# Kernel tuning notes

Hardware: AMD Instinct MI355X
Metric: run time of the kernel (lower is better)

## Reference

```python
import jax, jax.numpy as jnp
import numpy as np

HDIM = 4
P = 2 ** HDIM  # 16 hypercube nodes


def build_dense_weight(hweight, out_features, in_features):
    # hweight: [hdim+1, P, ob, ib]; assemble dense [out_features, in_features]
    ob = out_features // P
    ib = in_features // P
    i = jnp.arange(P)
    w = jnp.zeros((P, P, ob, ib), dtype=hweight.dtype)
    # diagonal blocks: w[i, i] = hweight[0, i]
    w = w.at[i, i].set(hweight[0])
    # hypercube neighbor blocks: w[i ^ (1<<d), i] = hweight[d+1, i]
    for d in range(HDIM):
        j = i ^ (1 << d)
        w = w.at[j, i].set(hweight[d + 1])
    # permute (0,2,1,3) then reshape -> [out_features, in_features]
    w = jnp.transpose(w, (0, 2, 1, 3)).reshape(out_features, in_features)
    return w


def setup_inputs() -> dict:
    key = jax.random.key(0)
    k1, k2, k3 = jax.random.split(key, 3)
    in_features, out_features = 4096, 4096
    ob = out_features // P
    ib = in_features // P
    x = jax.random.normal(k1, (8192, in_features), dtype=jnp.float32)
    # kaiming-uniform-like scale for the block weights
    bound_w = 1.0 / np.sqrt(ib)
    hweight = jax.random.uniform(k2, (HDIM + 1, P, ob, ib), dtype=jnp.float32,
                                 minval=-bound_w, maxval=bound_w)
    bound_b = 1.0 / np.sqrt(in_features * (HDIM + 1))
    hbias = jax.random.uniform(k3, (out_features,), dtype=jnp.float32,
                               minval=-bound_b, maxval=bound_b)
    return {"x": x, "hweight": hweight, "hbias": hbias}


def reference(x, hweight, hbias):
    out_features = hweight.shape[1] * hweight.shape[2]
    in_features = hweight.shape[1] * hweight.shape[3]
    w = build_dense_weight(hweight, out_features, in_features)
    # F.linear(x, w, b) = x @ w.T + b
    return x @ w.T + hbias
```

## Files before the change

### kernel.cpp

```cpp
#include <hip/hip_runtime.h>

typedef __attribute__((ext_vector_type(8))) short short8;
typedef __attribute__((ext_vector_type(4))) float f32x4;

#define INF 4096
#define NKT 40
#define BUFB 24576

#define AS1 __attribute__((address_space(1)))
#define AS3 __attribute__((address_space(3)))

__device__ __forceinline__ unsigned short f2bf(float f) {
    unsigned int u = __float_as_uint(f);
    u += 0x7FFFu + ((u >> 16) & 1u);
    return (unsigned short)(u >> 16);
}

__device__ __forceinline__ void gl_lds16(const unsigned short* g, void* l) {
    __builtin_amdgcn_global_load_lds((const AS1 void*)g, (AS3 void*)l, 16, 0, 0);
}

__device__ __forceinline__ int swz(int b) { return b ^ ((b >> 3) & 0x30); }

__global__ __launch_bounds__(256)
void cvt_bf16(const float* __restrict__ x, const float* __restrict__ hw,
              unsigned short* __restrict__ xb, unsigned short* __restrict__ wb)
{
    const long long NX = 8192LL * 4096;
    const long long NW = 5LL * 16 * 256 * 256;
    const long long total8 = (NX + NW) / 8;
    for (long long i = (long long)blockIdx.x * 256 + threadIdx.x; i < total8;
         i += (long long)gridDim.x * 256) {
        long long e = i * 8;
        const float* src;
        unsigned short* dst;
        long long off;
        if (e < NX) { src = x;  dst = xb; off = e; }
        else        { src = hw; dst = wb; off = e - NX; }
        float4 f0 = *(const float4*)(src + off);
        float4 f1 = *(const float4*)(src + off + 4);
        ushort4 u0, u1;
        u0.x = f2bf(f0.x); u0.y = f2bf(f0.y); u0.z = f2bf(f0.z); u0.w = f2bf(f0.w);
        u1.x = f2bf(f1.x); u1.y = f2bf(f1.y); u1.z = f2bf(f1.z); u1.w = f2bf(f1.w);
        *(ushort4*)(dst + off)     = u0;
        *(ushort4*)(dst + off + 4) = u1;
    }
}

__global__ __launch_bounds__(256, 2)
void hcl_gemm4(const unsigned short* __restrict__ xb,
               const unsigned short* __restrict__ wb,
               const float* __restrict__ hb,
               float* __restrict__ out)
{
    extern __shared__ unsigned short lds[];

    const int tid  = threadIdx.x;
    const int lane = tid & 63;
    const int wave = tid >> 6;
    const int ln15 = lane & 15;
    const int hi   = lane >> 4;

    const int bm0 = blockIdx.x * 128;
    const int p   = blockIdx.y;

    int rj[4], cj[4];
    #pragma unroll
    for (int j = 0; j < 4; ++j) {
        int g = swz(j * 4096 + tid * 16);
        rj[j] = g >> 6;
        cj[j] = (g & 63) >> 1;
    }

    int offA[8], offB[4];
    #pragma unroll
    for (int mf = 0; mf < 8; ++mf)
        offA[mf] = swz((mf * 16 + ln15) * 64 + hi * 16);
    #pragma unroll
    for (int nf = 0; nf < 4; ++nf)
        offB[nf] = swz((wave * 64 + nf * 16 + ln15) * 64 + hi * 16);

    f32x4 acc[8][4] = {};

    auto STAGE = [&](int kt, int buf) {
        const int t = kt >> 3;
        const int s = p ^ ((1 << t) >> 1);
        const unsigned short* ga = xb + (size_t)bm0 * INF + s * 256 + (kt & 7) * 32;
        const unsigned short* gb = wb + ((size_t)(t * 16 + s) << 16) + (kt & 7) * 32;
        char* lb = (char*)lds + buf * BUFB + wave * 1024;
        gl_lds16(ga + (size_t)rj[0] * INF + cj[0], lb);
        gl_lds16(ga + (size_t)rj[1] * INF + cj[1], lb + 4096);
        gl_lds16(gb + (size_t)rj[0] * 256 + cj[0], lb + 8192);
        gl_lds16(gb + (size_t)rj[1] * 256 + cj[1], lb + 8192 + 4096);
        gl_lds16(gb + (size_t)rj[2] * 256 + cj[2], lb + 8192 + 8192);
        gl_lds16(gb + (size_t)rj[3] * 256 + cj[3], lb + 8192 + 12288);
    };

    auto COMPUTE = [&](int buf) {
        const char* LA = (const char*)lds + buf * BUFB;
        const char* LB = LA + 8192;
        short8 fa[8], fb[4];
        #pragma unroll
        for (int nf = 0; nf < 4; ++nf) fb[nf] = *(const short8*)(LB + offB[nf]);
        #pragma unroll
        for (int mf = 0; mf < 8; ++mf) fa[mf] = *(const short8*)(LA + offA[mf]);
        __builtin_amdgcn_s_setprio(1);
        #pragma unroll
        for (int mf = 0; mf < 8; ++mf)
            #pragma unroll
            for (int nf = 0; nf < 4; ++nf)
                acc[mf][nf] = __builtin_amdgcn_mfma_f32_16x16x32_bf16(
                    fa[mf], fb[nf], acc[mf][nf], 0, 0, 0);
        __builtin_amdgcn_s_setprio(0);
    };

    STAGE(0, 0);
    STAGE(1, 1);

    for (int kt = 0; kt < NKT - 2; ++kt) {
        STAGE(kt + 2, (kt + 2) % 3);
        asm volatile("s_waitcnt vmcnt(12)");
        __builtin_amdgcn_s_barrier();
        __builtin_amdgcn_sched_barrier(0);
        COMPUTE(kt % 3);
        __builtin_amdgcn_s_barrier();
        __builtin_amdgcn_sched_barrier(0);
    }
    asm volatile("s_waitcnt vmcnt(6)");
    __builtin_amdgcn_s_barrier();
    __builtin_amdgcn_sched_barrier(0);
    COMPUTE((NKT - 2) % 3);
    __builtin_amdgcn_s_barrier();
    asm volatile("s_waitcnt vmcnt(0)");
    __builtin_amdgcn_s_barrier();
    __builtin_amdgcn_sched_barrier(0);
    COMPUTE((NKT - 1) % 3);

    const int col0 = p * 256 + wave * 64;
    #pragma unroll
    for (int nf = 0; nf < 4; ++nf) {
        const int col = col0 + nf * 16 + ln15;
        const float bias = hb[col];
        #pragma unroll
        for (int mf = 0; mf < 8; ++mf) {
            #pragma unroll
            for (int r = 0; r < 4; ++r) {
                const int row = bm0 + mf * 16 + hi * 4 + r;
                out[(size_t)row * 4096 + col] = acc[mf][nf][r] + bias;
            }
        }
    }
}

__global__ __launch_bounds__(256)
void hcl_mfma_fused(const float* __restrict__ x,
                    const float* __restrict__ hw,
                    const float* __restrict__ hb,
                    float* __restrict__ out)
{
    __shared__ unsigned short As[128][32];
    __shared__ unsigned short Bs[128][32];

    const int tid  = threadIdx.x;
    const int lane = tid & 63;
    const int wave = tid >> 6;
    const int wr   = wave >> 1, wc = wave & 1;

    const int bm0 = blockIdx.x * 128;
    const int p   = blockIdx.y >> 1;
    const int nh  = blockIdx.y & 1;

    f32x4 acc[4][4] = {};

    const int srow = tid >> 3;
    const int scol = (tid & 7) * 4;

    #pragma unroll
    for (int t = 0; t < 5; ++t) {
        const int mask = (t == 0) ? 0 : (1 << (t - 1));
        const int s = p ^ mask;
        const float* xchunk = x  + (size_t)bm0 * INF + s * 256;
        const float* wchunk = hw + ((size_t)(t * 16 + s) * 256 + nh * 128) * 256;

        for (int k8 = 0; k8 < 8; ++k8) {
            const int kc = k8 * 32;
            #pragma unroll
            for (int i = 0; i < 4; ++i) {
                const int row = i * 32 + srow;
                float4 fa = *(const float4*)(xchunk + (size_t)row * INF + kc + scol);
                float4 fb = *(const float4*)(wchunk + (size_t)row * 256 + kc + scol);
                ushort4 ua, ub;
                ua.x = f2bf(fa.x); ua.y = f2bf(fa.y);
                ua.z = f2bf(fa.z); ua.w = f2bf(fa.w);
                ub.x = f2bf(fb.x); ub.y = f2bf(fb.y);
                ub.z = f2bf(fb.z); ub.w = f2bf(fb.w);
                *(ushort4*)&As[row][scol] = ua;
                *(ushort4*)&Bs[row][scol] = ub;
            }
            __syncthreads();

            short8 a[4], b[4];
            #pragma unroll
            for (int mi = 0; mi < 4; ++mi)
                a[mi] = *(const short8*)&As[wr * 64 + mi * 16 + (lane & 15)][(lane >> 4) * 8];
            #pragma unroll
            for (int nj = 0; nj < 4; ++nj)
                b[nj] = *(const short8*)&Bs[wc * 64 + nj * 16 + (lane & 15)][(lane >> 4) * 8];

            #pragma unroll
            for (int mi = 0; mi < 4; ++mi)
                #pragma unroll
                for (int nj = 0; nj < 4; ++nj)
                    acc[mi][nj] = __builtin_amdgcn_mfma_f32_16x16x32_bf16(
                        a[mi], b[nj], acc[mi][nj], 0, 0, 0);

            __syncthreads();
        }
    }

    const int col0 = p * 256 + nh * 128 + wc * 64;
    #pragma unroll
    for (int nj = 0; nj < 4; ++nj) {
        const int col = col0 + nj * 16 + (lane & 15);
        const float bias = hb[col];
        #pragma unroll
        for (int mi = 0; mi < 4; ++mi) {
            #pragma unroll
            for (int r = 0; r < 4; ++r) {
                const int row = bm0 + wr * 64 + mi * 16 + (lane >> 4) * 4 + r;
                out[(size_t)row * 4096 + col] = acc[mi][nj][r] + bias;
            }
        }
    }
}

extern "C" void kernel_launch(void* const* d_in, const int* in_sizes, int n_in,
                              void* d_out, int out_size, void* d_ws, size_t ws_size,
                              hipStream_t stream) {
    const float* x  = (const float*)d_in[0];
    const float* hw = (const float*)d_in[1];
    const float* hb = (const float*)d_in[2];
    float* out = (float*)d_out;

    const size_t NX = 8192ull * 4096;
    const size_t NW = 5ull * 16 * 256 * 256;
    const size_t need = (NX + NW) * sizeof(unsigned short);

    if (ws_size >= need) {
        unsigned short* xb = (unsigned short*)d_ws;
        unsigned short* wb = xb + NX;
        cvt_bf16<<<2048, 256, 0, stream>>>(x, hw, xb, wb);
        dim3 grid(8192 / 128, 16);
        hcl_gemm4<<<grid, 256, 3 * BUFB, stream>>>(xb, wb, hb, out);
    } else {
        dim3 grid(8192 / 128, 32);
        hcl_mfma_fused<<<grid, 256, 0, stream>>>(x, hw, hb, out);
    }
}
```

Measured before the change: 155.0 us.

## Add 256x256-tile 8-wave GEMM with quadrant ping-pong LDS schedule

Introduces a new GEMM kernel using 512 threads and 256x256 output tiles with a 64-wide K step and a double-buffered 128KB LDS layout. Fragment loads and MFMA blocks are interleaved per quadrant with async global-to-LDS staging. The goal is more operand reuse per loaded byte and better overlap of loads with matrix math. In exchange it needs a large dynamic LDS allocation, holds only one block per CU, and the register pressure from the launch bounds may cause spills. The old kernel is kept as a fallback if the LDS attribute cannot be set.

```diff
diff --git a/kernel.cpp b/kernel.cpp
--- a/kernel.cpp
+++ b/kernel.cpp
@@ -4,8 +4,6 @@
 typedef __attribute__((ext_vector_type(4))) float f32x4;
 
 #define INF 4096
-#define NKT 40
-#define BUFB 24576
 
 #define AS1 __attribute__((address_space(1)))
 #define AS3 __attribute__((address_space(3)))
@@ -20,7 +18,12 @@
     __builtin_amdgcn_global_load_lds((const AS1 void*)g, (AS3 void*)l, 16, 0, 0);
 }
 
-__device__ __forceinline__ int swz(int b) { return b ^ ((b >> 3) & 0x30); }
+__device__ __forceinline__ int swz7(int b) { return b ^ ((b >> 3) & 0x70); }
+__device__ __forceinline__ int swz6(int b) { return b ^ ((b >> 3) & 0x30); }
+
+#define BAR()   __builtin_amdgcn_s_barrier()
+#define SB0()   __builtin_amdgcn_sched_barrier(0)
+#define LGKM0() { asm volatile("s_waitcnt lgkmcnt(0)" ::: "memory"); __builtin_amdgcn_sched_barrier(0); }
 
 __global__ __launch_bounds__(256)
 void cvt_bf16(const float* __restrict__ x, const float* __restrict__ hw,
@@ -47,13 +50,144 @@
     }
 }
 
+__global__ __launch_bounds__(512, 2)
+void hcl_gemm8p(const unsigned short* __restrict__ xb,
+                const unsigned short* __restrict__ wb,
+                const float* __restrict__ hb,
+                float* __restrict__ out)
+{
+    extern __shared__ char lds[];
+
+    const int tid  = threadIdx.x;
+    const int lane = tid & 63;
+    const int wave = tid >> 6;
+    const int wr   = wave >> 2;
+    const int wcn  = wave & 3;
+    const int ln15 = lane & 15;
+    const int hi   = lane >> 4;
+
+    const int bm0 = blockIdx.x * 256;
+    const int p   = blockIdx.y;
+
+    int offA[8], offB[4];
+    #pragma unroll
+    for (int mf = 0; mf < 8; ++mf)
+        offA[mf] = wr * 16384 + swz7((mf * 16 + ln15) * 128 + hi * 16);
+    #pragma unroll
+    for (int nf = 0; nf < 4; ++nf)
+        offB[nf] = 32768 + (wcn >> 1) * 16384 +
+                   swz7(((wcn & 1) * 64 + nf * 16 + ln15) * 128 + hi * 16);
+
+    int srow[2], skcol[2];
+    #pragma unroll
+    for (int j = 0; j < 2; ++j) {
+        int L = swz7(j * 8192 + tid * 16);
+        srow[j]  = L >> 7;
+        skcol[j] = (L & 127) >> 1;
+    }
+
+    f32x4 acc[8][4] = {};
+
+    auto STAGE = [&](int kt, int reg) {
+        if (kt >= 20) return;
+        const int t  = kt >> 2;
+        const int s  = p ^ ((1 << t) >> 1);
+        const int k0 = (kt & 3) * 64;
+        char* dst = lds + (kt & 1) * 65536 + reg * 16384 + tid * 16;
+        if (reg < 2) {
+            const unsigned short* g = xb + (size_t)(bm0 + reg * 128) * INF + s * 256 + k0;
+            gl_lds16(g + (size_t)srow[0] * INF + skcol[0], dst);
+            gl_lds16(g + (size_t)srow[1] * INF + skcol[1], dst + 8192);
+        } else {
+            const unsigned short* g = wb + ((size_t)(t * 16 + s) << 16) + (reg - 2) * 32768 + k0;
+            gl_lds16(g + (size_t)srow[0] * 256 + skcol[0], dst);
+            gl_lds16(g + (size_t)srow[1] * 256 + skcol[1], dst + 8192);
+        }
+    };
+
+    short8 fa[8], fb[4];
+    auto LDA = [&](int qm, int buf) {
+        const char* L = lds + buf * 65536;
+        #pragma unroll
+        for (int m = 0; m < 4; ++m) {
+            fa[m * 2 + 0] = *(const short8*)(L + offA[qm * 4 + m]);
+            fa[m * 2 + 1] = *(const short8*)(L + (offA[qm * 4 + m] ^ 64));
+        }
+    };
+    auto LDB = [&](int qn, int buf) {
+        const char* L = lds + buf * 65536;
+        #pragma unroll
+        for (int n = 0; n < 2; ++n) {
+            fb[n * 2 + 0] = *(const short8*)(L + offB[qn * 2 + n]);
+            fb[n * 2 + 1] = *(const short8*)(L + (offB[qn * 2 + n] ^ 64));
+        }
+    };
+    auto MM = [&](int qm, int qn) {
+        __builtin_amdgcn_s_setprio(1);
+        #pragma unroll
+        for (int m = 0; m < 4; ++m)
+            #pragma unroll
+            for (int n = 0; n < 2; ++n)
+                #pragma unroll
+                for (int ks = 0; ks < 2; ++ks)
+                    acc[qm * 4 + m][qn * 2 + n] = __builtin_amdgcn_mfma_f32_16x16x32_bf16(
+                        fa[m * 2 + ks], fb[n * 2 + ks], acc[qm * 4 + m][qn * 2 + n], 0, 0, 0);
+        __builtin_amdgcn_s_setprio(0);
+    };
+
+    STAGE(0, 0); STAGE(0, 1); STAGE(0, 2); STAGE(0, 3); STAGE(1, 0);
+    asm volatile("s_waitcnt vmcnt(2)" ::: "memory");
+    BAR(); SB0();
+
+    for (int i = 0; i < 10; ++i) {
+        const int ktB = 2 * i + 1;
+        const int ktN = 2 * i + 2;
+        LDA(0, 0); LDB(0, 0); STAGE(ktB, 1);
+        BAR(); LGKM0(); MM(0, 0); BAR(); SB0();
+        LDB(1, 0); STAGE(ktB, 2);
+        BAR(); LGKM0(); MM(0, 1); BAR(); SB0();
+        LDA(1, 0); STAGE(ktB, 3);
+        BAR(); LGKM0(); MM(1, 1); BAR(); SB0();
+        LDB(0, 0); STAGE(ktN, 0);
+        if (i < 9) { asm volatile("s_waitcnt vmcnt(2)" ::: "memory"); }
+        else       { asm volatile("s_waitcnt vmcnt(0)" ::: "memory"); }
+        BAR(); LGKM0(); MM(1, 0); BAR(); SB0();
+        LDA(0, 1); LDB(0, 1); STAGE(ktN, 1);
+        BAR(); LGKM0(); MM(0, 0); BAR(); SB0();
+        LDB(1, 1); STAGE(ktN, 2);
+        BAR(); LGKM0(); MM(0, 1); BAR(); SB0();
+        LDA(1, 1); STAGE(ktN, 3);
+        BAR(); LGKM0(); MM(1, 1); BAR(); SB0();
+        LDB(0, 1); STAGE(ktN + 1, 0);
+        if (i < 9) { asm volatile("s_waitcnt vmcnt(2)" ::: "memory"); }
+        BAR(); LGKM0(); MM(1, 0); BAR(); SB0();
+    }
+
+    const int col0 = p * 256 + wcn * 64;
+    #pragma unroll
+    for (int nf = 0; nf < 4; ++nf) {
+        const int col = col0 + nf * 16 + ln15;
+        const float bias = hb[col];
+        #pragma unroll
+        for (int mf = 0; mf < 8; ++mf) {
+            #pragma unroll
+            for (int r = 0; r < 4; ++r) {
+                const int row = bm0 + wr * 128 + mf * 16 + hi * 4 + r;
+                out[(size_t)row * 4096 + col] = acc[mf][nf][r] + bias;
+            }
+        }
+    }
+}
+
+#define NKT4 40
+#define BUFB4 24576
 __global__ __launch_bounds__(256, 2)
 void hcl_gemm4(const unsigned short* __restrict__ xb,
                const unsigned short* __restrict__ wb,
                const float* __restrict__ hb,
                float* __restrict__ out)
 {
-    extern __shared__ unsigned short lds[];
+    extern __shared__ unsigned short lds4[];
 
     const int tid  = threadIdx.x;
     const int lane = tid & 63;
@@ -67,7 +201,7 @@
     int rj[4], cj[4];
     #pragma unroll
     for (int j = 0; j < 4; ++j) {
-        int g = swz(j * 4096 + tid * 16);
+        int g = swz6(j * 4096 + tid * 16);
         rj[j] = g >> 6;
         cj[j] = (g & 63) >> 1;
     }
@@ -75,10 +209,10 @@
     int offA[8], offB[4];
     #pragma unroll
     for (int mf = 0; mf < 8; ++mf)
-        offA[mf] = swz((mf * 16 + ln15) * 64 + hi * 16);
+        offA[mf] = swz6((mf * 16 + ln15) * 64 + hi * 16);
     #pragma unroll
     for (int nf = 0; nf < 4; ++nf)
-        offB[nf] = swz((wave * 64 + nf * 16 + ln15) * 64 + hi * 16);
+        offB[nf] = swz6((wave * 64 + nf * 16 + ln15) * 64 + hi * 16);
 
     f32x4 acc[8][4] = {};
 
@@ -87,7 +221,7 @@
         const int s = p ^ ((1 << t) >> 1);
         const unsigned short* ga = xb + (size_t)bm0 * INF + s * 256 + (kt & 7) * 32;
         const unsigned short* gb = wb + ((size_t)(t * 16 + s) << 16) + (kt & 7) * 32;
-        char* lb = (char*)lds + buf * BUFB + wave * 1024;
+        char* lb = (char*)lds4 + buf * BUFB4 + wave * 1024;
         gl_lds16(ga + (size_t)rj[0] * INF + cj[0], lb);
         gl_lds16(ga + (size_t)rj[1] * INF + cj[1], lb + 4096);
         gl_lds16(gb + (size_t)rj[0] * 256 + cj[0], lb + 8192);
@@ -97,7 +231,7 @@
     };
 
     auto COMPUTE = [&](int buf) {
-        const char* LA = (const char*)lds + buf * BUFB;
+        const char* LA = (const char*)lds4 + buf * BUFB4;
         const char* LB = LA + 8192;
         short8 fa[8], fb[4];
         #pragma unroll
@@ -116,25 +250,20 @@
 
     STAGE(0, 0);
     STAGE(1, 1);
-
-    for (int kt = 0; kt < NKT - 2; ++kt) {
+    for (int kt = 0; kt < NKT4 - 2; ++kt) {
         STAGE(kt + 2, (kt + 2) % 3);
-        asm volatile("s_waitcnt vmcnt(12)");
-        __builtin_amdgcn_s_barrier();
-        __builtin_amdgcn_sched_barrier(0);
+        asm volatile("s_waitcnt vmcnt(12)" ::: "memory");
+        BAR(); SB0();
         COMPUTE(kt % 3);
-        __builtin_amdgcn_s_barrier();
-        __builtin_amdgcn_sched_barrier(0);
-    }
-    asm volatile("s_waitcnt vmcnt(6)");
-    __builtin_amdgcn_s_barrier();
-    __builtin_amdgcn_sched_barrier(0);
-    COMPUTE((NKT - 2) % 3);
-    __builtin_amdgcn_s_barrier();
-    asm volatile("s_waitcnt vmcnt(0)");
-    __builtin_amdgcn_s_barrier();
-    __builtin_amdgcn_sched_barrier(0);
-    COMPUTE((NKT - 1) % 3);
+        BAR(); SB0();
+    }
+    asm volatile("s_waitcnt vmcnt(6)" ::: "memory");
+    BAR(); SB0();
+    COMPUTE((NKT4 - 2) % 3);
+    BAR(); SB0();
+    asm volatile("s_waitcnt vmcnt(0)" ::: "memory");
+    BAR(); SB0();
+    COMPUTE((NKT4 - 1) % 3);
 
     const int col0 = p * 256 + wave * 64;
     #pragma unroll
@@ -250,8 +379,16 @@
         unsigned short* xb = (unsigned short*)d_ws;
         unsigned short* wb = xb + NX;
         cvt_bf16<<<2048, 256, 0, stream>>>(x, hw, xb, wb);
-        dim3 grid(8192 / 128, 16);
-        hcl_gemm4<<<grid, 256, 3 * BUFB, stream>>>(xb, wb, hb, out);
+        hipError_t e = hipFuncSetAttribute((const void*)hcl_gemm8p,
+                                           hipFuncAttributeMaxDynamicSharedMemorySize,
+                                           131072);
+        if (e == hipSuccess) {
+            dim3 grid(8192 / 256, 16);
+            hcl_gemm8p<<<grid, 512, 131072, stream>>>(xb, wb, hb, out);
+        } else {
+            dim3 grid(8192 / 128, 16);
+            hcl_gemm4<<<grid, 256, 3 * BUFB4, stream>>>(xb, wb, hb, out);
+        }
     } else {
         dim3 grid(8192 / 128, 32);
         hcl_mfma_fused<<<grid, 256, 0, stream>>>(x, hw, hb, out);
```

Result: slower. 225.6 us (+45.6%).

## Load B fragments directly from global memory and stage only A through LDS

Applied to the files above, without the earlier changes.

Rewrites the hypercube GEMM main loop so each wave reads its weight (B) MFMA fragments straight from global memory into registers, and only the activation (A) tile goes through LDS via global_load_lds. The K step per iteration doubles to 64, which halves the loop trip count and the barriers. The LDS swizzle is widened to match the 128-byte rows, and the LDS buffers become a static allocation. The aim is to cut LDS traffic and synchronisation per MFMA, at the cost of exposing global-load latency on B and relying on L2 to serve B reuse across blocks.

```diff
diff --git a/kernel.cpp b/kernel.cpp
--- a/kernel.cpp
+++ b/kernel.cpp
@@ -4,8 +4,6 @@
 typedef __attribute__((ext_vector_type(4))) float f32x4;
 
 #define INF 4096
-#define NKT 40
-#define BUFB 24576
 
 #define AS1 __attribute__((address_space(1)))
 #define AS3 __attribute__((address_space(3)))
@@ -20,7 +18,10 @@
     __builtin_amdgcn_global_load_lds((const AS1 void*)g, (AS3 void*)l, 16, 0, 0);
 }
 
-__device__ __forceinline__ int swz(int b) { return b ^ ((b >> 3) & 0x30); }
+__device__ __forceinline__ int swz7(int b) { return b ^ ((b >> 3) & 0x70); }
+
+#define BAR()   __builtin_amdgcn_s_barrier()
+#define SB0()   __builtin_amdgcn_sched_barrier(0)
 
 __global__ __launch_bounds__(256)
 void cvt_bf16(const float* __restrict__ x, const float* __restrict__ hw,
@@ -48,12 +49,12 @@
 }
 
 __global__ __launch_bounds__(256, 2)
-void hcl_gemm4(const unsigned short* __restrict__ xb,
-               const unsigned short* __restrict__ wb,
-               const float* __restrict__ hb,
-               float* __restrict__ out)
+void hcl_gbd(const unsigned short* __restrict__ xb,
+             const unsigned short* __restrict__ wb,
+             const float* __restrict__ hb,
+             float* __restrict__ out)
 {
-    extern __shared__ unsigned short lds[];
+    __shared__ char lds[3 * 16384];
 
     const int tid  = threadIdx.x;
     const int lane = tid & 63;
@@ -64,77 +65,90 @@
     const int bm0 = blockIdx.x * 128;
     const int p   = blockIdx.y;
 
-    int rj[4], cj[4];
+    int offA[8];
+    #pragma unroll
+    for (int mf = 0; mf < 8; ++mf)
+        offA[mf] = swz7((mf * 16 + ln15) * 128 + hi * 16);
+
+    int srow[4], skcol[4];
     #pragma unroll
     for (int j = 0; j < 4; ++j) {
-        int g = swz(j * 4096 + tid * 16);
-        rj[j] = g >> 6;
-        cj[j] = (g & 63) >> 1;
-    }
-
-    int offA[8], offB[4];
-    #pragma unroll
-    for (int mf = 0; mf < 8; ++mf)
-        offA[mf] = swz((mf * 16 + ln15) * 64 + hi * 16);
-    #pragma unroll
-    for (int nf = 0; nf < 4; ++nf)
-        offB[nf] = swz((wave * 64 + nf * 16 + ln15) * 64 + hi * 16);
+        int L = swz7(j * 4096 + tid * 16);
+        srow[j]  = L >> 7;
+        skcol[j] = (L & 127) >> 1;
+    }
+
+    const unsigned short* gB = wb + (size_t)(wave * 64 + ln15) * 256 + hi * 8;
 
     f32x4 acc[8][4] = {};
 
-    auto STAGE = [&](int kt, int buf) {
-        const int t = kt >> 3;
+    auto STAGE = [&](int kt) {
+        if (kt >= 20) return;
+        const int t  = kt >> 2;
+        const int s  = p ^ ((1 << t) >> 1);
+        const int k0 = (kt & 3) * 64;
+        const unsigned short* ga = xb + (size_t)bm0 * INF + s * 256 + k0;
+        char* dst = lds + (kt % 3) * 16384 + tid * 16;
+        gl_lds16(ga + (size_t)srow[0] * INF + skcol[0], dst);
+        gl_lds16(ga + (size_t)srow[1] * INF + skcol[1], dst + 4096);
+        gl_lds16(ga + (size_t)srow[2] * INF + skcol[2], dst + 8192);
+        gl_lds16(ga + (size_t)srow[3] * INF + skcol[3], dst + 12288);
+    };
+
+    short8 fa[8], fb[8];
+    auto LDA = [&](int qm, const char* L) {
+        #pragma unroll
+        for (int m = 0; m < 4; ++m) {
+            fa[m * 2 + 0] = *(const short8*)(L + offA[qm * 4 + m]);
+            fa[m * 2 + 1] = *(const short8*)(L + (offA[qm * 4 + m] ^ 64));
+        }
+    };
+    auto MM0 = [&](int qm) {
+        __builtin_amdgcn_s_setprio(1);
+        #pragma unroll
+        for (int m = 0; m < 4; ++m)
+            #pragma unroll
+            for (int n = 0; n < 2; ++n)
+                #pragma unroll
+                for (int ks = 0; ks < 2; ++ks)
+                    acc[qm * 4 + m][n] = __builtin_amdgcn_mfma_f32_16x16x32_bf16(
+                        fa[m * 2 + ks], fb[n * 2 + ks], acc[qm * 4 + m][n], 0, 0, 0);
+        __builtin_amdgcn_s_setprio(0);
+    };
+    auto MM1 = [&](int qm) {
+        __builtin_amdgcn_s_setprio(1);
+        #pragma unroll
+        for (int m = 0; m < 4; ++m)
+            #pragma unroll
+            for (int n = 0; n < 2; ++n)
+                #pragma unroll
+                for (int ks = 0; ks < 2; ++ks)
+                    acc[qm * 4 + m][2 + n] = __builtin_amdgcn_mfma_f32_16x16x32_bf16(
+                        fa[m * 2 + ks], fb[4 + n * 2 + ks], acc[qm * 4 + m][2 + n], 0, 0, 0);
+        __builtin_amdgcn_s_setprio(0);
+    };
+
+    STAGE(0); STAGE(1);
+    asm volatile("s_waitcnt vmcnt(4)" ::: "memory");
+    BAR(); SB0();
+
+    for (int kt = 0; kt < 20; ++kt) {
+        const int t = kt >> 2;
         const int s = p ^ ((1 << t) >> 1);
-        const unsigned short* ga = xb + (size_t)bm0 * INF + s * 256 + (kt & 7) * 32;
-        const unsigned short* gb = wb + ((size_t)(t * 16 + s) << 16) + (kt & 7) * 32;
-        char* lb = (char*)lds + buf * BUFB + wave * 1024;
-        gl_lds16(ga + (size_t)rj[0] * INF + cj[0], lb);
-        gl_lds16(ga + (size_t)rj[1] * INF + cj[1], lb + 4096);
-        gl_lds16(gb + (size_t)rj[0] * 256 + cj[0], lb + 8192);
-        gl_lds16(gb + (size_t)rj[1] * 256 + cj[1], lb + 8192 + 4096);
-        gl_lds16(gb + (size_t)rj[2] * 256 + cj[2], lb + 8192 + 8192);
-        gl_lds16(gb + (size_t)rj[3] * 256 + cj[3], lb + 8192 + 12288);
-    };
-
-    auto COMPUTE = [&](int buf) {
-        const char* LA = (const char*)lds + buf * BUFB;
-        const char* LB = LA + 8192;
-        short8 fa[8], fb[4];
-        #pragma unroll
-        for (int nf = 0; nf < 4; ++nf) fb[nf] = *(const short8*)(LB + offB[nf]);
-        #pragma unroll
-        for (int mf = 0; mf < 8; ++mf) fa[mf] = *(const short8*)(LA + offA[mf]);
-        __builtin_amdgcn_s_setprio(1);
-        #pragma unroll
-        for (int mf = 0; mf < 8; ++mf)
-            #pragma unroll
-            for (int nf = 0; nf < 4; ++nf)
-                acc[mf][nf] = __builtin_amdgcn_mfma_f32_16x16x32_bf16(
-                    fa[mf], fb[nf], acc[mf][nf], 0, 0, 0);
-        __builtin_amdgcn_s_setprio(0);
-    };
-
-    STAGE(0, 0);
-    STAGE(1, 1);
-
-    for (int kt = 0; kt < NKT - 2; ++kt) {
-        STAGE(kt + 2, (kt + 2) % 3);
-        asm volatile("s_waitcnt vmcnt(12)");
-        __builtin_amdgcn_s_barrier();
-        __builtin_amdgcn_sched_barrier(0);
-        COMPUTE(kt % 3);
-        __builtin_amdgcn_s_barrier();
-        __builtin_amdgcn_sched_barrier(0);
-    }
-    asm volatile("s_waitcnt vmcnt(6)");
-    __builtin_amdgcn_s_barrier();
-    __builtin_amdgcn_sched_barrier(0);
-    COMPUTE((NKT - 2) % 3);
-    __builtin_amdgcn_s_barrier();
-    asm volatile("s_waitcnt vmcnt(0)");
-    __builtin_amdgcn_s_barrier();
-    __builtin_amdgcn_sched_barrier(0);
-    COMPUTE((NKT - 1) % 3);
+        const size_t tOff = ((size_t)(t * 16 + s) << 16) + (kt & 3) * 64;
+        #pragma unroll
+        for (int nf = 0; nf < 4; ++nf)
+            #pragma unroll
+            for (int ks = 0; ks < 2; ++ks)
+                fb[nf * 2 + ks] = *(const short8*)(gB + tOff + nf * 4096 + ks * 32);
+        SB0();
+        STAGE(kt + 2);
+        SB0();
+        const char* L = lds + (kt % 3) * 16384;
+        LDA(0, L); MM0(0); MM1(0);
+        LDA(1, L); MM0(1); MM1(1);
+        BAR(); SB0();
+    }
 
     const int col0 = p * 256 + wave * 64;
     #pragma unroll
@@ -251,7 +265,7 @@
         unsigned short* wb = xb + NX;
         cvt_bf16<<<2048, 256, 0, stream>>>(x, hw, xb, wb);
         dim3 grid(8192 / 128, 16);
-        hcl_gemm4<<<grid, 256, 3 * BUFB, stream>>>(xb, wb, hb, out);
+        hcl_gbd<<<grid, 256, 0, stream>>>(xb, wb, hb, out);
     } else {
         dim3 grid(8192 / 128, 32);
         hcl_mfma_fused<<<grid, 256, 0, stream>>>(x, hw, hb, out);
```

After: 162.4 us. 4.8% more time.

## Shrink GEMM tile to 128x128 with 2x2 wave grid and XCD-aware block remap

Applied to the files above, without the earlier changes.

Replaces the 128x256 block tile with a 128x128 tile split across a 2x2 wave grid, halving LDS per stage and allowing three blocks per CU. Blocks are launched on a 1D grid and remapped so that consecutive blocks on each XCD share weight and activation panels. Per-block stage loads drop from six to four and wait counts are adjusted to match. The smaller tile raises occupancy and doubles the grid size, but lowers arithmetic intensity per LDS byte and means each activation tile is loaded by twice as many blocks.

```diff
diff --git a/kernel.cpp b/kernel.cpp
--- a/kernel.cpp
+++ b/kernel.cpp
@@ -5,7 +5,7 @@
 
 #define INF 4096
 #define NKT 40
-#define BUFB 24576
+#define BUFB 16384
 
 #define AS1 __attribute__((address_space(1)))
 #define AS3 __attribute__((address_space(3)))
@@ -20,7 +20,10 @@
     __builtin_amdgcn_global_load_lds((const AS1 void*)g, (AS3 void*)l, 16, 0, 0);
 }
 
-__device__ __forceinline__ int swz(int b) { return b ^ ((b >> 3) & 0x30); }
+__device__ __forceinline__ int swz6(int b) { return b ^ ((b >> 3) & 0x30); }
+
+#define BAR()   __builtin_amdgcn_s_barrier()
+#define SB0()   __builtin_amdgcn_sched_barrier(0)
 
 __global__ __launch_bounds__(256)
 void cvt_bf16(const float* __restrict__ x, const float* __restrict__ hw,
@@ -47,106 +50,105 @@
     }
 }
 
-__global__ __launch_bounds__(256, 2)
-void hcl_gemm4(const unsigned short* __restrict__ xb,
-               const unsigned short* __restrict__ wb,
-               const float* __restrict__ hb,
-               float* __restrict__ out)
+__global__ __launch_bounds__(256, 3)
+void hcl_g128(const unsigned short* __restrict__ xb,
+              const unsigned short* __restrict__ wb,
+              const float* __restrict__ hb,
+              float* __restrict__ out)
 {
-    extern __shared__ unsigned short lds[];
+    __shared__ char lds[3 * BUFB];
 
     const int tid  = threadIdx.x;
     const int lane = tid & 63;
     const int wave = tid >> 6;
+    const int wr   = wave >> 1;
+    const int wc   = wave & 1;
     const int ln15 = lane & 15;
     const int hi   = lane >> 4;
 
-    const int bm0 = blockIdx.x * 128;
-    const int p   = blockIdx.y;
-
-    int rj[4], cj[4];
-    #pragma unroll
-    for (int j = 0; j < 4; ++j) {
-        int g = swz(j * 4096 + tid * 16);
-        rj[j] = g >> 6;
-        cj[j] = (g & 63) >> 1;
-    }
-
-    int offA[8], offB[4];
-    #pragma unroll
-    for (int mf = 0; mf < 8; ++mf)
-        offA[mf] = swz((mf * 16 + ln15) * 64 + hi * 16);
+    const int newid = (blockIdx.x & 7) * 256 + (blockIdx.x >> 3);
+    const int col_i = newid >> 6;
+    const int bm0   = (newid & 63) * 128;
+    const int p     = col_i >> 1;
+    const int nh    = col_i & 1;
+
+    int offA[4], offB[4];
+    #pragma unroll
+    for (int mf = 0; mf < 4; ++mf)
+        offA[mf] = swz6((wr * 64 + mf * 16 + ln15) * 64 + hi * 16);
     #pragma unroll
     for (int nf = 0; nf < 4; ++nf)
-        offB[nf] = swz((wave * 64 + nf * 16 + ln15) * 64 + hi * 16);
-
-    f32x4 acc[8][4] = {};
+        offB[nf] = 8192 + swz6((wc * 64 + nf * 16 + ln15) * 64 + hi * 16);
+
+    int rj[2], cj[2];
+    #pragma unroll
+    for (int j = 0; j < 2; ++j) {
+        int L = swz6(j * 4096 + tid * 16);
+        rj[j] = L >> 6;
+        cj[j] = (L & 63) >> 1;
+    }
+
+    f32x4 acc[4][4] = {};
 
     auto STAGE = [&](int kt, int buf) {
-        const int t = kt >> 3;
-        const int s = p ^ ((1 << t) >> 1);
-        const unsigned short* ga = xb + (size_t)bm0 * INF + s * 256 + (kt & 7) * 32;
-        const unsigned short* gb = wb + ((size_t)(t * 16 + s) << 16) + (kt & 7) * 32;
-        char* lb = (char*)lds + buf * BUFB + wave * 1024;
+        if (kt >= NKT) return;
+        const int t  = kt >> 3;
+        const int s  = p ^ ((1 << t) >> 1);
+        const int k0 = (kt & 7) * 32;
+        const unsigned short* ga = xb + (size_t)bm0 * INF + s * 256 + k0;
+        const unsigned short* gb = wb + ((size_t)(t * 16 + s) << 16) + nh * 128 * 256 + k0;
+        char* lb = lds + buf * BUFB + tid * 16;
         gl_lds16(ga + (size_t)rj[0] * INF + cj[0], lb);
         gl_lds16(ga + (size_t)rj[1] * INF + cj[1], lb + 4096);
         gl_lds16(gb + (size_t)rj[0] * 256 + cj[0], lb + 8192);
         gl_lds16(gb + (size_t)rj[1] * 256 + cj[1], lb + 8192 + 4096);
-        gl_lds16(gb + (size_t)rj[2] * 256 + cj[2], lb + 8192 + 8192);
-        gl_lds16(gb + (size_t)rj[3] * 256 + cj[3], lb + 8192 + 12288);
     };
 
     auto COMPUTE = [&](int buf) {
-        const char* LA = (const char*)lds + buf * BUFB;
-        const char* LB = LA + 8192;
-        short8 fa[8], fb[4];
-        #pragma unroll
-        for (int nf = 0; nf < 4; ++nf) fb[nf] = *(const short8*)(LB + offB[nf]);
-        #pragma unroll
-        for (int mf = 0; mf < 8; ++mf) fa[mf] = *(const short8*)(LA + offA[mf]);
+        const char* L = lds + buf * BUFB;
+        short8 fa[4], fb[4];
+        #pragma unroll
+        for (int nf = 0; nf < 4; ++nf) fb[nf] = *(const short8*)(L + offB[nf]);
+        #pragma unroll
+        for (int mf = 0; mf < 4; ++mf) fa[mf] = *(const short8*)(L + offA[mf]);
         __builtin_amdgcn_s_setprio(1);
         #pragma unroll
-        for (int mf = 0; mf < 8; ++mf)
-            #pragma unroll
-            for (int nf = 0; nf < 4; ++nf)
-                acc[mf][nf] = __builtin_amdgcn_mfma_f32_16x16x32_bf16(
-                    fa[mf], fb[nf], acc[mf][nf], 0, 0, 0);
+        for (int mi = 0; mi < 4; ++mi)
+            #pragma unroll
+            for (int nj = 0; nj < 4; ++nj)
+                acc[mi][nj] = __builtin_amdgcn_mfma_f32_16x16x32_bf16(
+                    fa[mi], fb[nj], acc[mi][nj], 0, 0, 0);
         __builtin_amdgcn_s_setprio(0);
     };
 
     STAGE(0, 0);
     STAGE(1, 1);
-
     for (int kt = 0; kt < NKT - 2; ++kt) {
         STAGE(kt + 2, (kt + 2) % 3);
-        asm volatile("s_waitcnt vmcnt(12)");
-        __builtin_amdgcn_s_barrier();
-        __builtin_amdgcn_sched_barrier(0);
+        asm volatile("s_waitcnt vmcnt(8)" ::: "memory");
+        BAR(); SB0();
         COMPUTE(kt % 3);
-        __builtin_amdgcn_s_barrier();
-        __builtin_amdgcn_sched_barrier(0);
-    }
-    asm volatile("s_waitcnt vmcnt(6)");
-    __builtin_amdgcn_s_barrier();
-    __builtin_amdgcn_sched_barrier(0);
+        BAR(); SB0();
+    }
+    asm volatile("s_waitcnt vmcnt(4)" ::: "memory");
+    BAR(); SB0();
     COMPUTE((NKT - 2) % 3);
-    __builtin_amdgcn_s_barrier();
-    asm volatile("s_waitcnt vmcnt(0)");
-    __builtin_amdgcn_s_barrier();
-    __builtin_amdgcn_sched_barrier(0);
+    BAR(); SB0();
+    asm volatile("s_waitcnt vmcnt(0)" ::: "memory");
+    BAR(); SB0();
     COMPUTE((NKT - 1) % 3);
 
-    const int col0 = p * 256 + wave * 64;
-    #pragma unroll
-    for (int nf = 0; nf < 4; ++nf) {
-        const int col = col0 + nf * 16 + ln15;
+    const int col0 = p * 256 + nh * 128 + wc * 64;
+    #pragma unroll
+    for (int nj = 0; nj < 4; ++nj) {
+        const int col = col0 + nj * 16 + ln15;
         const float bias = hb[col];
         #pragma unroll
-        for (int mf = 0; mf < 8; ++mf) {
+        for (int mi = 0; mi < 4; ++mi) {
             #pragma unroll
             for (int r = 0; r < 4; ++r) {
-                const int row = bm0 + mf * 16 + hi * 4 + r;
-                out[(size_t)row * 4096 + col] = acc[mf][nf][r] + bias;
+                const int row = bm0 + wr * 64 + mi * 16 + hi * 4 + r;
+                out[(size_t)row * 4096 + col] = acc[mi][nj][r] + bias;
             }
         }
     }
@@ -250,8 +252,7 @@
         unsigned short* xb = (unsigned short*)d_ws;
         unsigned short* wb = xb + NX;
         cvt_bf16<<<2048, 256, 0, stream>>>(x, hw, xb, wb);
-        dim3 grid(8192 / 128, 16);
-        hcl_gemm4<<<grid, 256, 3 * BUFB, stream>>>(xb, wb, hb, out);
+        hcl_g128<<<2048, 256, 0, stream>>>(xb, wb, hb, out);
     } else {
         dim3 grid(8192 / 128, 32);
         hcl_mfma_fused<<<grid, 256, 0, stream>>>(x, hw, hb, out);
```

Measured after the change: 178.4 us. 1.15x slower.
